# Optimization experiments

Hardware: AMD Instinct MI355X
Metric: run time of the kernel (lower is better)

The kernel has to match this reference:

```python
import jax, jax.numpy as jnp
import numpy as np

B, N, C, H, HD, HH, WW, K, ALPHA = 8, 4096, 256, 8, 32, 64, 64, 5, 4.0


def setup_inputs() -> dict:
    key = jax.random.key(0)
    ks = jax.random.split(key, 6)
    return {
        "x": jax.random.normal(ks[0], (B, N, C), jnp.float32),
        "W_qg": jax.random.normal(ks[1], (C, 2 * C), jnp.float32) * 0.02,
        "W_kv": jax.random.normal(ks[2], (C, 2 * C), jnp.float32) * 0.02,
        "W_proj": jax.random.normal(ks[3], (C, C), jnp.float32) * 0.02,
        "b_proj": jnp.zeros((C,), jnp.float32),
        "dwc_w": jax.random.normal(ks[4], (HD, 1, K, K), jnp.float32) * 0.05,
        "dwc_b": jnp.zeros((HD,), jnp.float32),
        "power_p": jnp.zeros((1, H, 1, HD), jnp.float32),
    }


def _safe_pow(x, p):
    # x >= 0 (post-relu). 0**p == 0 for p > 0; guard base so grads stay finite.
    xs = jnp.where(x > 0, x, 1.0)
    return jnp.where(x > 0, xs ** p, 0.0)


def reference(x, W_qg, W_kv, W_proj, b_proj, dwc_w, dwc_b, power_p):
    qg = x @ W_qg                                  # (B,N,2C)
    q, g = qg[..., :C], qg[..., C:]
    kv = x @ W_kv                                  # (B,N,2C)
    k = kv[..., :C].reshape(B, N, H, HD).transpose(0, 2, 1, 3)   # (B,H,N,hd)
    v = kv[..., C:].reshape(B, N, H, HD).transpose(0, 2, 1, 3)
    q = q.reshape(B, N, H, HD).transpose(0, 2, 1, 3)

    power = 1.0 + ALPHA * jax.nn.sigmoid(power_p)  # (1,H,1,hd)
    # x_s = q_pos@kv_s + q_neg@kv_s = (q_pos+q_neg)@kv_s, kv_s = (k_pos+k_neg)^T v_s
    q_sum = _safe_pow(jax.nn.relu(q), power) + _safe_pow(jax.nn.relu(-q), power)
    k_sum = _safe_pow(jax.nn.relu(k), power) + _safe_pow(jax.nn.relu(-k), power)

    v_s, v_o = v[..., : HD // 2], v[..., HD // 2 :]
    kv_s = jnp.einsum('bhnd,bhne->bhde', k_sum, v_s)
    kv_o = jnp.einsum('bhnd,bhne->bhde', k_sum, v_o)
    x_s = jnp.einsum('bhnd,bhde->bhne', q_sum, kv_s)
    x_o = jnp.einsum('bhnd,bhde->bhne', q_sum, kv_o)
    x_att = jnp.concatenate([x_s, x_o], -1).transpose(0, 2, 1, 3).reshape(B, N, C)

    # depthwise conv branch: exact layout replication of torch permute/reshape chain
    v_img = v.transpose(0, 2, 1, 3).reshape(B * H, HD, HH, WW)
    pad = K // 2
    v_loc = jax.lax.conv_general_dilated(
        v_img, dwc_w, (1, 1), [(pad, pad), (pad, pad)],
        feature_group_count=HD,
        dimension_numbers=('NCHW', 'OIHW', 'NCHW')) + dwc_b[None, :, None, None]
    v_loc = v_loc.reshape(B, H, HD, N).transpose(0, 2, 1, 3).reshape(B, C, N).transpose(0, 2, 1)

    return ((x_att + v_loc) * g) @ W_proj + b_proj
```

## Files before the change

kernel.cpp:

```cpp
#include <hip/hip_runtime.h>
#include <hip/hip_bf16.h>
#include <math.h>

#define B_ 8
#define N_ 4096
#define C_ 256
#define H_ 8
#define HD_ 32
#define BN_ (B_ * N_)
#define E_ ((size_t)BN_ * C_)

typedef __attribute__((ext_vector_type(8))) short short8;
typedef __attribute__((ext_vector_type(4))) float f32x4;

__device__ __forceinline__ float b2f(__hip_bfloat16 x) { return __bfloat162float(x); }

__device__ __forceinline__ void gl_lds16(const void* gp, void* lp) {
    __builtin_amdgcn_global_load_lds(
        (const __attribute__((address_space(1))) unsigned int*)gp,
        (__attribute__((address_space(3))) unsigned int*)lp,
        16, 0, 0);
}

__device__ __forceinline__ float fast_abspow(float v, float p) {
    float av = fabsf(v);
    return (av > 0.f) ? __builtin_amdgcn_exp2f(p * __builtin_amdgcn_logf(av)) : 0.f;
}

__device__ __forceinline__ float bf_lo(unsigned u) { return __uint_as_float(u << 16); }
__device__ __forceinline__ float bf_hi(unsigned u) { return __uint_as_float(u & 0xffff0000u); }
__device__ __forceinline__ unsigned short f2bfbits(float f) {
    __hip_bfloat16 h = __float2bfloat16(f);
    return *(unsigned short*)&h;
}
__device__ __forceinline__ unsigned pack2(float lo, float hi) {
    return (unsigned)f2bfbits(lo) | ((unsigned)f2bfbits(hi) << 16);
}

__global__ __launch_bounds__(256) void cvt_all(
    const float* __restrict__ x, const float* __restrict__ Wqg,
    const float* __restrict__ Wkv, const float* __restrict__ Wp,
    const float* __restrict__ pp,
    __hip_bfloat16* __restrict__ xb, __hip_bfloat16* __restrict__ Wt1,
    __hip_bfloat16* __restrict__ Wt2, float* __restrict__ powers,
    float* __restrict__ kv_mat2)
{
    int t = threadIdx.x;
    int bid0 = blockIdx.x;
    if (bid0 < 4096) {
        size_t i = ((size_t)bid0 * 256 + t) * 8;
        float4 a = *(const float4*)&x[i];
        float4 b = *(const float4*)&x[i + 4];
        uint4 o = {pack2(a.x, a.y), pack2(a.z, a.w), pack2(b.x, b.y), pack2(b.z, b.w)};
        *(uint4*)&xb[i] = o;
        return;
    }
    int bid = bid0 - 4096;
    if (bid == 80) {
        powers[t] = 1.0f + 4.0f / (1.0f + expf(-pp[t]));
        return;
    }
    if (bid >= 81) {
        ((float4*)kv_mat2)[(size_t)(bid - 81) * 256 + t] = (float4){0.f, 0.f, 0.f, 0.f};
        return;
    }
    __shared__ float tile[64][65];
    const float* src;
    __hip_bfloat16* dst;
    int scols, tr, tc, dn0;
    if (bid < 32)      { src = Wqg; scols = 512; tr = bid >> 3;        tc = bid & 7;        dst = Wt1; dn0 = tc * 64; }
    else if (bid < 64) { src = Wkv; scols = 512; tr = (bid - 32) >> 3; tc = (bid - 32) & 7; dst = Wt1; dn0 = 512 + tc * 64; }
    else               { src = Wp;  scols = 256; tr = (bid - 64) >> 2; tc = (bid - 64) & 3; dst = Wt2; dn0 = tc * 64; }
    int tx = t & 63, ty = t >> 6;
    #pragma unroll
    for (int i = 0; i < 16; i++) {
        int r = ty + i * 4;
        tile[r][tx] = src[(size_t)(tr * 64 + r) * scols + tc * 64 + tx];
    }
    __syncthreads();
    #pragma unroll
    for (int i = 0; i < 16; i++) {
        int n_local = ty + i * 4;
        dst[(size_t)(dn0 + n_local) * 256 + tr * 64 + tx] = __float2bfloat16(tile[tx][n_local]);
    }
}

__global__ __launch_bounds__(256) void gemm1_mfma(
    const __hip_bfloat16* __restrict__ xb, const __hip_bfloat16* __restrict__ Wt1,
    const float* __restrict__ powers,
    __hip_bfloat16* __restrict__ q16, __hip_bfloat16* __restrict__ k16,
    __hip_bfloat16* __restrict__ g16, __hip_bfloat16* __restrict__ v16)
{
    __shared__ __align__(16) unsigned short ABs[128 * 128];
    unsigned short* As = ABs;
    unsigned short* Bs = ABs + 128 * 64;
    int t = threadIdx.x;
    int w = t >> 6, l = t & 63;
    int bswz = (blockIdx.x & 7) * 256 + (blockIdx.x >> 3);
    int row0 = (bswz >> 3) * 128;
    int colb = bswz & 7;
    int col0 = colb * 128;
    int wm = (w >> 1) * 64, wn = (w & 1) * 64;
    int lane15 = l & 15, quad = l >> 4;
    int sr8 = l >> 3;
    int sc = ((l & 7) ^ sr8) * 8;
    int r7 = lane15 & 7;

    f32x4 acc[4][4];
    #pragma unroll
    for (int mi = 0; mi < 4; mi++)
        #pragma unroll
        for (int ni = 0; ni < 4; ni++) acc[mi][ni] = (f32x4){0.f, 0.f, 0.f, 0.f};

    for (int k0 = 0; k0 < 256; k0 += 64) {
        #pragma unroll
        for (int j = 0; j < 4; j++) {
            int rowl = j * 32 + w * 8 + sr8;
            gl_lds16(&xb[(size_t)(row0 + rowl) * 256 + k0 + sc],
                     &As[(j * 32 + w * 8) * 64]);
            gl_lds16(&Wt1[(size_t)(col0 + rowl) * 256 + k0 + sc],
                     &Bs[(j * 32 + w * 8) * 64]);
        }
        __syncthreads();
        #pragma unroll
        for (int kh = 0; kh < 2; kh++) {
            int cs_k = ((kh * 4 + quad) ^ r7) * 8;
            short8 a[4], b[4];
            #pragma unroll
            for (int mi = 0; mi < 4; mi++)
                a[mi] = *(const short8*)&As[(wm + mi * 16 + lane15) * 64 + cs_k];
            #pragma unroll
            for (int ni = 0; ni < 4; ni++)
                b[ni] = *(const short8*)&Bs[(wn + ni * 16 + lane15) * 64 + cs_k];
            #pragma unroll
            for (int mi = 0; mi < 4; mi++)
                #pragma unroll
                for (int ni = 0; ni < 4; ni++)
                    acc[mi][ni] = __builtin_amdgcn_mfma_f32_16x16x32_bf16(a[mi], b[ni], acc[mi][ni], 0, 0, 0);
        }
        __syncthreads();
    }

    int region = colb >> 1;
    bool dopow = (region == 0) || (region == 2);
    __hip_bfloat16* dst = (region == 0) ? q16 : (region == 1) ? g16 : (region == 2) ? k16 : v16;
    int cbase = col0 & 255;
    #pragma unroll
    for (int mi = 0; mi < 4; mi++) {
        #pragma unroll
        for (int ni = 0; ni < 4; ni++) {
            int rowb = wm + mi * 16 + quad * 4;
            int coll = wn + ni * 16 + lane15;
            float p = powers[cbase + coll];
            int cchunk = coll >> 3, cin = coll & 7;
            #pragma unroll
            for (int r = 0; r < 4; r++) {
                int rl = rowb + r;
                float v = acc[mi][ni][r];
                float o = dopow ? fast_abspow(v, p) : v;
                ABs[rl * 128 + ((cchunk ^ (rl & 15)) << 3) + cin] = f2bfbits(o);
            }
        }
    }
    __syncthreads();
    #pragma unroll
    for (int j = 0; j < 8; j++) {
        int g = j * 256 + t;
        int rl = g >> 4, chunk = g & 15;
        uint4 vv = *(const uint4*)&ABs[rl * 128 + ((chunk ^ (rl & 15)) << 3)];
        *(uint4*)&dst[(size_t)(row0 + rl) * 256 + cbase + chunk * 8] = vv;
    }
}

__global__ __launch_bounds__(256) void kvconv_kernel(
    const __hip_bfloat16* __restrict__ k16, const __hip_bfloat16* __restrict__ v16,
    float* __restrict__ kv_mat2,
    const float* __restrict__ w, const float* __restrict__ bias,
    __hip_bfloat16* __restrict__ vloc)
{
    __shared__ __align__(16) unsigned char smraw[18560];
    int t = threadIdx.x;

    if (blockIdx.x < 512) {
        unsigned short (*KV)[32][136] = (unsigned short (*)[32][136])smraw;
        int w_ = t >> 6, l = t & 63;
        int lane15 = l & 15, quad = l >> 4;
        int bid = blockIdx.x;
        int pair = bid >> 3, seg = bid & 7;
        int b = pair >> 3, h = pair & 7;
        int nloc = t & 127, cs = (t >> 7) * 16;

        f32x4 acc[2][2];
        #pragma unroll
        for (int di = 0; di < 2; di++)
            #pragma unroll
            for (int ei = 0; ei < 2; ei++) acc[di][ei] = (f32x4){0.f, 0.f, 0.f, 0.f};

        const size_t base = (size_t)b * N_ * 256 + h * 32 + cs;
        for (int c4 = 0; c4 < 4; c4++) {
            int n0 = seg * 512 + c4 * 128;
            const uint4* kp = (const uint4*)(k16 + base + (size_t)(n0 + nloc) * 256);
            uint4 ka = kp[0], kb = kp[1];
            const uint4* vp = (const uint4*)(v16 + base + (size_t)(n0 + nloc) * 256);
            uint4 va = vp[0], vb = vp[1];
            __syncthreads();
            unsigned kw[8] = {ka.x, ka.y, ka.z, ka.w, kb.x, kb.y, kb.z, kb.w};
            unsigned vw[8] = {va.x, va.y, va.z, va.w, vb.x, vb.y, vb.z, vb.w};
            #pragma unroll
            for (int j = 0; j < 8; j++) {
                KV[0][cs + 2 * j][nloc]     = (unsigned short)(kw[j] & 0xffffu);
                KV[0][cs + 2 * j + 1][nloc] = (unsigned short)(kw[j] >> 16);
                KV[1][cs + 2 * j][nloc]     = (unsigned short)(vw[j] & 0xffffu);
                KV[1][cs + 2 * j + 1][nloc] = (unsigned short)(vw[j] >> 16);
            }
            __syncthreads();
            int nb = w_ * 32 + quad * 8;
            short8 a[2], bb[2];
            #pragma unroll
            for (int di = 0; di < 2; di++)
                a[di] = *(const short8*)&KV[0][di * 16 + lane15][nb];
            #pragma unroll
            for (int ei = 0; ei < 2; ei++)
                bb[ei] = *(const short8*)&KV[1][ei * 16 + lane15][nb];
            #pragma unroll
            for (int di = 0; di < 2; di++)
                #pragma unroll
                for (int ei = 0; ei < 2; ei++)
                    acc[di][ei] = __builtin_amdgcn_mfma_f32_16x16x32_bf16(a[di], bb[ei], acc[di][ei], 0, 0, 0);
        }

        __syncthreads();
        float* red = (float*)smraw;
        #pragma unroll
        for (int di = 0; di < 2; di++)
            #pragma unroll
            for (int ei = 0; ei < 2; ei++) {
                int e = ei * 16 + lane15;
                #pragma unroll
                for (int r = 0; r < 4; r++) {
                    int d = di * 16 + quad * 4 + r;
                    red[w_ * 1056 + e * 33 + d] = acc[di][ei][r];
                }
            }
        __syncthreads();
        #pragma unroll
        for (int j = 0; j < 4; j++) {
            int o = j * 256 + t;
            int e = o >> 5, d = o & 31;
            float s = red[e * 33 + d] + red[1056 + e * 33 + d]
                    + red[2112 + e * 33 + d] + red[3168 + e * 33 + d];
            atomicAdd(&kv_mat2[(size_t)b * 8192 + e * 256 + h * 32 + d], s);
        }
        return;
    }

    float* img = (float*)smraw;
    float* wl  = (float*)(smraw + 18432);
    int gid = blockIdx.x - 512;
    int DD = gid & 31;
    if (t < 128) {
        int row = t >> 1, side = (t & 1) * 68;
        *(float4*)&img[row * 72 + side] = (float4){0.f, 0.f, 0.f, 0.f};
    }
    if (t < 25) wl[t] = w[DD * 25 + t];
    {
        int row = t >> 2, colb = (t & 3) * 16;
        const uint4* src = (const uint4*)(v16 + (size_t)gid * 4096 + row * 64 + colb);
        uint4 u0 = src[0], u1 = src[1];
        float4* d = (float4*)&img[row * 72 + 4 + colb];
        d[0] = (float4){bf_lo(u0.x), bf_hi(u0.x), bf_lo(u0.y), bf_hi(u0.y)};
        d[1] = (float4){bf_lo(u0.z), bf_hi(u0.z), bf_lo(u0.w), bf_hi(u0.w)};
        d[2] = (float4){bf_lo(u1.x), bf_hi(u1.x), bf_lo(u1.y), bf_hi(u1.y)};
        d[3] = (float4){bf_lo(u1.z), bf_hi(u1.z), bf_lo(u1.w), bf_hi(u1.w)};
    }
    __syncthreads();
    float bs = bias[DD];
    int x0 = (t & 15) * 4, yb = t >> 4;
    #pragma unroll
    for (int s = 0; s < 4; s++) {
        int y = yb + s * 16;
        float a0 = bs, a1 = bs, a2 = bs, a3 = bs;
        #pragma unroll
        for (int ky = 0; ky < 5; ky++) {
            int row = y + ky - 2;
            if (row < 0 || row >= 64) continue;
            const float* rp = &img[row * 72 + x0];
            float4 w0 = *(const float4*)rp;
            float4 w1 = *(const float4*)(rp + 4);
            float4 w2 = *(const float4*)(rp + 8);
            float win[12] = {w0.x, w0.y, w0.z, w0.w, w1.x, w1.y, w1.z, w1.w,
                             w2.x, w2.y, w2.z, w2.w};
            #pragma unroll
            for (int kx = 0; kx < 5; kx++) {
                float wt = wl[ky * 5 + kx];
                a0 += wt * win[2 + kx];
                a1 += wt * win[3 + kx];
                a2 += wt * win[4 + kx];
                a3 += wt * win[5 + kx];
            }
        }
        unsigned lo = pack2(a0, a1);
        unsigned hi = pack2(a2, a3);
        *(uint2*)(vloc + (size_t)gid * 4096 + y * 64 + x0) = (uint2){lo, hi};
    }
}

#define A2P 264
__global__ __launch_bounds__(256) void att_gemm2(
    const __hip_bfloat16* __restrict__ q16, const float* __restrict__ kv_mat2,
    const __hip_bfloat16* __restrict__ vloc, const __hip_bfloat16* __restrict__ g16,
    const __hip_bfloat16* __restrict__ Wt2, const float* __restrict__ bp,
    float* __restrict__ out)
{
    __shared__ __align__(16) unsigned short QA[64 * A2P];
    __shared__ __align__(16) unsigned short Bs[256 * 32];
    int t = threadIdx.x;
    int w = t >> 6, l = t & 63;
    int r0 = blockIdx.x * 64;
    int b = r0 >> 12, n0 = r0 & 4095;
    int lane15 = l & 15, quad = l >> 4;
    int h0 = w * 2;

    {
        const uint4* qsrc = (const uint4*)(q16 + (size_t)(r0 + (t >> 2)) * 256 + (t & 3) * 64);
        uint4* qdst = (uint4*)&QA[(t >> 2) * A2P + (t & 3) * 64];
        #pragma unroll
        for (int j = 0; j < 8; j++) qdst[j] = qsrc[j];
    }
    __syncthreads();

    short8 afr[4][2];
    #pragma unroll
    for (int m = 0; m < 4; m++)
        #pragma unroll
        for (int hh = 0; hh < 2; hh++)
            afr[m][hh] = *(const short8*)&QA[(m * 16 + lane15) * A2P + (h0 + hh) * 32 + quad * 8];

    short8 bfr[2][2];
    #pragma unroll
    for (int hh = 0; hh < 2; hh++) {
        #pragma unroll
        for (int nt = 0; nt < 2; nt++) {
            const float4* kp = (const float4*)(kv_mat2 + (size_t)b * 8192 +
                (size_t)(nt * 16 + lane15) * 256 + (h0 + hh) * 32 + quad * 8);
            float4 ka = kp[0], kb = kp[1];
            short8 bb;
            bb[0] = (short)f2bfbits(ka.x); bb[1] = (short)f2bfbits(ka.y);
            bb[2] = (short)f2bfbits(ka.z); bb[3] = (short)f2bfbits(ka.w);
            bb[4] = (short)f2bfbits(kb.x); bb[5] = (short)f2bfbits(kb.y);
            bb[6] = (short)f2bfbits(kb.z); bb[7] = (short)f2bfbits(kb.w);
            bfr[hh][nt] = bb;
        }
    }

    f32x4 ac[4][2][2];
    #pragma unroll
    for (int m = 0; m < 4; m++)
        #pragma unroll
        for (int hh = 0; hh < 2; hh++)
            #pragma unroll
            for (int nt = 0; nt < 2; nt++)
                ac[m][hh][nt] = __builtin_amdgcn_mfma_f32_16x16x32_bf16(
                    afr[m][hh], bfr[hh][nt], (f32x4){0.f, 0.f, 0.f, 0.f}, 0, 0, 0);

    #pragma unroll
    for (int m = 0; m < 4; m++) {
        #pragma unroll
        for (int hh = 0; hh < 2; hh++) {
            #pragma unroll
            for (int nt = 0; nt < 2; nt++) {
                int col = (h0 + hh) * 32 + nt * 16 + lane15;
                int rowb = m * 16 + quad * 4;
                size_t img = ((size_t)((b * 8 + (col & 7)) * 32 + (col >> 3))) * 4096 + n0 + rowb;
                uint2 vv = *(const uint2*)(vloc + img);
                float vl[4] = {bf_lo(vv.x), bf_hi(vv.x), bf_lo(vv.y), bf_hi(vv.y)};
                #pragma unroll
                for (int i = 0; i < 4; i++) {
                    float gg = b2f(g16[(size_t)(r0 + rowb + i) * 256 + col]);
                    float val = (ac[m][hh][nt][i] + vl[i]) * gg;
                    QA[(rowb + i) * A2P + col] = f2bfbits(val);
                }
            }
        }
    }

    int wm = (w & 1) * 32, wn = (w >> 1) * 128;
    f32x4 acc2[2][8];
    #pragma unroll
    for (int mi = 0; mi < 2; mi++)
        #pragma unroll
        for (int ni = 0; ni < 8; ni++) acc2[mi][ni] = (f32x4){0.f, 0.f, 0.f, 0.f};

    for (int k0 = 0; k0 < 256; k0 += 32) {
        __syncthreads();
        #pragma unroll
        for (int j = 0; j < 4; j++) {
            int rowl = j * 64 + w * 16 + (l >> 2);
            int gchunk = (l & 3) ^ ((l >> 3) & 3);
            gl_lds16(&Wt2[(size_t)rowl * 256 + k0 + gchunk * 8],
                     &Bs[(j * 64 + w * 16) * 32]);
        }
        __syncthreads();
        short8 a[2], bb[8];
        #pragma unroll
        for (int mi = 0; mi < 2; mi++)
            a[mi] = *(const short8*)&QA[(wm + mi * 16 + lane15) * A2P + k0 + quad * 8];
        #pragma unroll
        for (int ni = 0; ni < 8; ni++) {
            int r = wn + ni * 16 + lane15;
            bb[ni] = *(const short8*)&Bs[r * 32 + ((quad ^ ((r >> 1) & 3)) << 3)];
        }
        #pragma unroll
        for (int mi = 0; mi < 2; mi++)
            #pragma unroll
            for (int ni = 0; ni < 8; ni++)
                acc2[mi][ni] = __builtin_amdgcn_mfma_f32_16x16x32_bf16(a[mi], bb[ni], acc2[mi][ni], 0, 0, 0);
    }

    #pragma unroll
    for (int mi = 0; mi < 2; mi++) {
        #pragma unroll
        for (int ni = 0; ni < 8; ni++) {
            int row = r0 + wm + mi * 16 + quad * 4;
            int col = wn + ni * 16 + lane15;
            float bv = bp[col];
            #pragma unroll
            for (int r = 0; r < 4; r++)
                out[(size_t)(row + r) * 256 + col] = acc2[mi][ni][r] + bv;
        }
    }
}

extern "C" void kernel_launch(void* const* d_in, const int* in_sizes, int n_in,
                              void* d_out, int out_size, void* d_ws, size_t ws_size,
                              hipStream_t stream) {
    const float* x      = (const float*)d_in[0];
    const float* W_qg   = (const float*)d_in[1];
    const float* W_kv   = (const float*)d_in[2];
    const float* W_proj = (const float*)d_in[3];
    const float* b_proj = (const float*)d_in[4];
    const float* dwc_w  = (const float*)d_in[5];
    const float* dwc_b  = (const float*)d_in[6];
    const float* pow_p  = (const float*)d_in[7];
    float* out = (float*)d_out;

    float* ws = (float*)d_ws;
    const size_t E = E_;
    __hip_bfloat16* q16  = (__hip_bfloat16*)ws;
    __hip_bfloat16* k16  = (__hip_bfloat16*)(ws + E / 2);
    __hip_bfloat16* g16  = (__hip_bfloat16*)(ws + E);
    __hip_bfloat16* v16  = (__hip_bfloat16*)(ws + 3 * E / 2);
    __hip_bfloat16* xb   = (__hip_bfloat16*)(ws + 2 * E);
    __hip_bfloat16* vl16 = (__hip_bfloat16*)(ws + 5 * E / 2);
    float* kv_mat2 = ws + 3 * E;
    __hip_bfloat16* Wt1 = (__hip_bfloat16*)(kv_mat2 + 65536);
    __hip_bfloat16* Wt2 = Wt1 + 262144;
    float* powers = (float*)(Wt2 + 65536);

    cvt_all<<<4096 + 81 + 64, 256, 0, stream>>>(x, W_qg, W_kv, W_proj, pow_p, xb, Wt1, Wt2, powers, kv_mat2);
    gemm1_mfma<<<2048, 256, 0, stream>>>(xb, Wt1, powers, q16, k16, g16, v16);
    kvconv_kernel<<<512 + 2048, 256, 0, stream>>>(k16, v16, kv_mat2, dwc_w, dwc_b, vl16);
    att_gemm2<<<512, 256, 0, stream>>>(q16, kv_mat2, vl16, g16, Wt2, b_proj, out);
}
```

Before: 173.2 us.

## Double-buffer gemm1 LDS tiles with k=32 stages to overlap loads and MFMA

Restructures the projection GEMM main loop from four single-buffered k=64 stages into eight k=32 stages that ping-pong between two LDS buffers. The next tile is prefetched via global_load_lds while MFMAs run on the current one, and the swizzle is changed to suit the narrower 32-element rows. This aims to hide global-load latency behind compute. The cost is twice as many barriers and smaller per-stage work. Correctness depends on the async LDS loads finishing before the barrier.

Result: no change. 171.3 us (-1.1%).

```diff
diff --git a/kernel.cpp b/kernel.cpp
--- a/kernel.cpp
+++ b/kernel.cpp
@@ -92,8 +92,6 @@
     __hip_bfloat16* __restrict__ g16, __hip_bfloat16* __restrict__ v16)
 {
     __shared__ __align__(16) unsigned short ABs[128 * 128];
-    unsigned short* As = ABs;
-    unsigned short* Bs = ABs + 128 * 64;
     int t = threadIdx.x;
     int w = t >> 6, l = t & 63;
     int bswz = (blockIdx.x & 7) * 256 + (blockIdx.x >> 3);
@@ -102,9 +100,8 @@
     int col0 = colb * 128;
     int wm = (w >> 1) * 64, wn = (w & 1) * 64;
     int lane15 = l & 15, quad = l >> 4;
-    int sr8 = l >> 3;
-    int sc = ((l & 7) ^ sr8) * 8;
-    int r7 = lane15 & 7;
+    int srow4 = l >> 2;
+    int sgc = ((l & 3) ^ ((l >> 3) & 3)) * 8;
 
     f32x4 acc[4][4];
     #pragma unroll
@@ -112,32 +109,48 @@
         #pragma unroll
         for (int ni = 0; ni < 4; ni++) acc[mi][ni] = (f32x4){0.f, 0.f, 0.f, 0.f};
 
-    for (int k0 = 0; k0 < 256; k0 += 64) {
-        #pragma unroll
-        for (int j = 0; j < 4; j++) {
-            int rowl = j * 32 + w * 8 + sr8;
-            gl_lds16(&xb[(size_t)(row0 + rowl) * 256 + k0 + sc],
-                     &As[(j * 32 + w * 8) * 64]);
-            gl_lds16(&Wt1[(size_t)(col0 + rowl) * 256 + k0 + sc],
-                     &Bs[(j * 32 + w * 8) * 64]);
-        }
-        __syncthreads();
-        #pragma unroll
-        for (int kh = 0; kh < 2; kh++) {
-            int cs_k = ((kh * 4 + quad) ^ r7) * 8;
-            short8 a[4], b[4];
-            #pragma unroll
-            for (int mi = 0; mi < 4; mi++)
-                a[mi] = *(const short8*)&As[(wm + mi * 16 + lane15) * 64 + cs_k];
+    #pragma unroll
+    for (int j = 0; j < 2; j++) {
+        int rowl = j * 64 + w * 16 + srow4;
+        gl_lds16(&xb[(size_t)(row0 + rowl) * 256 + sgc],
+                 &ABs[(j * 64 + w * 16) * 32]);
+        gl_lds16(&Wt1[(size_t)(col0 + rowl) * 256 + sgc],
+                 &ABs[8192 + (j * 64 + w * 16) * 32]);
+    }
+    __syncthreads();
+
+    for (int ti = 0; ti < 8; ti++) {
+        int cur = ti & 1;
+        if (ti < 7) {
+            int nxt = cur ^ 1;
+            int kn = (ti + 1) * 32;
+            #pragma unroll
+            for (int j = 0; j < 2; j++) {
+                int rowl = j * 64 + w * 16 + srow4;
+                gl_lds16(&xb[(size_t)(row0 + rowl) * 256 + kn + sgc],
+                         &ABs[nxt * 4096 + (j * 64 + w * 16) * 32]);
+                gl_lds16(&Wt1[(size_t)(col0 + rowl) * 256 + kn + sgc],
+                         &ABs[8192 + nxt * 4096 + (j * 64 + w * 16) * 32]);
+            }
+        }
+        const unsigned short* Ac = ABs + cur * 4096;
+        const unsigned short* Bc = ABs + 8192 + cur * 4096;
+        short8 a[4], b[4];
+        #pragma unroll
+        for (int mi = 0; mi < 4; mi++) {
+            int r = wm + mi * 16 + lane15;
+            a[mi] = *(const short8*)&Ac[r * 32 + ((quad ^ ((r >> 1) & 3)) << 3)];
+        }
+        #pragma unroll
+        for (int ni = 0; ni < 4; ni++) {
+            int r = wn + ni * 16 + lane15;
+            b[ni] = *(const short8*)&Bc[r * 32 + ((quad ^ ((r >> 1) & 3)) << 3)];
+        }
+        #pragma unroll
+        for (int mi = 0; mi < 4; mi++)
             #pragma unroll
             for (int ni = 0; ni < 4; ni++)
-                b[ni] = *(const short8*)&Bs[(wn + ni * 16 + lane15) * 64 + cs_k];
-            #pragma unroll
-            for (int mi = 0; mi < 4; mi++)
-                #pragma unroll
-                for (int ni = 0; ni < 4; ni++)
-                    acc[mi][ni] = __builtin_amdgcn_mfma_f32_16x16x32_bf16(a[mi], b[ni], acc[mi][ni], 0, 0, 0);
-        }
+                acc[mi][ni] = __builtin_amdgcn_mfma_f32_16x16x32_bf16(a[mi], b[ni], acc[mi][ni], 0, 0, 0);
         __syncthreads();
     }
 
```
